# Kernel optimization log

Measured on AMD Instinct MI355X. Metric: run time of the kernel, lower is better.

Reference implementation:

```python
import jax, jax.numpy as jnp
import numpy as np


def _euclidean_cdist(x, q):
    # torch.cdist with p=2: pairwise L2 distances, shape [B, Q]
    x2 = jnp.sum(x * x, axis=-1, keepdims=True)          # [B, 1]
    q2 = jnp.sum(q * q, axis=-1)[None, :]                # [1, Q]
    d2 = x2 + q2 - 2.0 * (x @ q.T)                        # [B, Q]
    return jnp.sqrt(jnp.maximum(d2, 0.0))


def setup_inputs() -> dict:
    key = jax.random.key(0)
    k1, k2 = jax.random.split(key)
    x = jax.random.normal(k1, (1024, 256), dtype=jnp.float32)
    queue = jax.random.normal(k2, (32768, 256), dtype=jnp.float32)
    return {"x": x, "queue": queue}


def reference(x, queue):
    # Queue update: concat then keep the newest max_size rows (queue assumed full)
    max_size = queue.shape[0]
    q = jnp.concatenate([queue, x], axis=0)[-max_size:]   # [Q, F]
    # Distance matrix + top-2 nearest (topk of negated distances)
    d = _euclidean_cdist(x, q)                            # [B, Q]
    _, idx = jax.lax.top_k(-d, 2)                         # [B, 2]
    # Second-nearest neighbor (first is the point itself, dist 0)
    return q[idx[:, 1]]                                   # [B, F]
```

## Files before the change

kernel.cpp:

```cpp
#include <hip/hip_runtime.h>
#include <stdint.h>

#define B_ROWS 1024
#define FEAT   256
#define QSZ    32768
#define SHIFT  1024
#define QX     (QSZ - B_ROWS)
#define NQB    (QSZ / 128)

typedef float  v4f __attribute__((ext_vector_type(4)));
typedef short  v8s __attribute__((ext_vector_type(8)));

struct Top2 { float m1; int j1; float m2; int j2; };

__device__ __forceinline__ bool better(float ma, int ja, float mb, int jb) {
    return (ma < mb) || (ma == mb && ja < jb);
}
__device__ __forceinline__ void t2_insert(Top2& t, float m, int j) {
    if (better(m, j, t.m1, t.j1)) { t.m2 = t.m1; t.j2 = t.j1; t.m1 = m; t.j1 = j; }
    else if (better(m, j, t.m2, t.j2)) { t.m2 = m; t.j2 = j; }
}
__device__ __forceinline__ void t2_merge(Top2& a, const Top2& b) {
    t2_insert(a, b.m1, b.j1); t2_insert(a, b.m2, b.j2);
}
__device__ __forceinline__ float4 t2_pack(const Top2& t) {
    return make_float4(t.m1, __int_as_float(t.j1), t.m2, __int_as_float(t.j2));
}
__device__ __forceinline__ Top2 t2_unpack(float4 v) {
    Top2 t; t.m1 = v.x; t.j1 = __float_as_int(v.y); t.m2 = v.z; t.j2 = __float_as_int(v.w);
    return t;
}
__device__ __forceinline__ Top2 t2_shfl_xor(const Top2& a, int mask) {
    Top2 o;
    o.m1 = __shfl_xor(a.m1, mask, 64);
    o.j1 = __shfl_xor(a.j1, mask, 64);
    o.m2 = __shfl_xor(a.m2, mask, 64);
    o.j2 = __shfl_xor(a.j2, mask, 64);
    return o;
}

__device__ __forceinline__ const float* q_row_ptr(int j, const float* x, const float* queue) {
    return (j < QX) ? (queue + (size_t)(j + SHIFT) * FEAT) : (x + (size_t)(j - QX) * FEAT);
}

__device__ __forceinline__ unsigned short f2bf(float f) {
    uint32_t u = __float_as_uint(f);
    uint32_t r = u + 0x7FFFu + ((u >> 16) & 1u);
    return (unsigned short)(r >> 16);
}

__device__ __forceinline__ void lds_load16(const void* g, void* l) {
    __builtin_amdgcn_global_load_lds(
        (const __attribute__((address_space(1))) uint32_t*)g,
        (__attribute__((address_space(3))) uint32_t*)l, 16, 0, 0);
}

__global__ __launch_bounds__(256) void convert_kernel(const float* __restrict__ x,
                                                      const float* __restrict__ queue,
                                                      unsigned short* __restrict__ q_bf,
                                                      float* __restrict__ q2) {
    int wave = threadIdx.x >> 6, lane = threadIdx.x & 63;
    int j = blockIdx.x * 4 + wave;
    const float4* row = (const float4*)q_row_ptr(j, x, queue);
    float4 v = row[lane];
    float s = v.x * v.x + v.y * v.y + v.z * v.z + v.w * v.w;
#pragma unroll
    for (int off = 32; off; off >>= 1) s += __shfl_xor(s, off, 64);
    if (lane == 0) q2[j] = s;
    ushort4 h;
    h.x = f2bf(v.x); h.y = f2bf(v.y); h.z = f2bf(v.z); h.w = f2bf(v.w);
    ((ushort4*)q_bf)[(size_t)j * 64 + lane] = h;
}

__global__ __launch_bounds__(256, 3) void nn_mfma(const unsigned short* __restrict__ q_bf,
                                                  const float* __restrict__ q2,
                                                  float4* __restrict__ partials) {
    __shared__ unsigned short As[128 * 64];
    __shared__ unsigned short Bs[128 * 64];

    const int t    = threadIdx.x;
    const int w    = t >> 6, lane = t & 63;
    const int wm   = w >> 1, wn = w & 1;
    const int quad = lane >> 4, l16 = lane & 15;
    const int gy   = blockIdx.x;
    const int gx   = blockIdx.y;

    const unsigned short* x_bf = q_bf + (size_t)QX * FEAT;

    v4f acc[4][4];
#pragma unroll
    for (int a = 0; a < 4; ++a)
#pragma unroll
        for (int b = 0; b < 4; ++b) acc[a][b] = (v4f)0.0f;

    const int srow = lane >> 3;
    const int sg   = (lane & 7) ^ (srow & 7);

    for (int c = 0; c < 4; ++c) {
        __syncthreads();
#pragma unroll
        for (int kk = 0; kk < 4; ++kk) {
            int row = w * 32 + kk * 8 + srow;
            const unsigned short* ga = x_bf + (size_t)(gx * 128 + row) * FEAT + c * 64 + sg * 8;
            const unsigned short* gb = q_bf + (size_t)(gy * 128 + row) * FEAT + c * 64 + sg * 8;
            lds_load16(ga, &As[(w * 32 + kk * 8) * 64]);
            lds_load16(gb, &Bs[(w * 32 + kk * 8) * 64]);
        }
        __syncthreads();
#pragma unroll
        for (int ks = 0; ks < 2; ++ks) {
            v8s fa[4], fb[4];
            const int goff  = (((ks * 4 + quad) ^ (l16 & 7)) << 4);
            const int abase = (wm * 64 + l16) * 128 + goff;
            const int bbase = (wn * 64 + l16) * 128 + goff;
#pragma unroll
            for (int tm = 0; tm < 4; ++tm)
                fa[tm] = *(const v8s*)((const char*)As + abase + tm * 2048);
#pragma unroll
            for (int tn = 0; tn < 4; ++tn)
                fb[tn] = *(const v8s*)((const char*)Bs + bbase + tn * 2048);
#pragma unroll
            for (int tm = 0; tm < 4; ++tm)
#pragma unroll
                for (int tn = 0; tn < 4; ++tn)
                    acc[tm][tn] = __builtin_amdgcn_mfma_f32_16x16x32_bf16(fa[tm], fb[tn], acc[tm][tn], 0, 0, 0);
        }
    }

    float q2v[4]; int jcol[4];
#pragma unroll
    for (int tn = 0; tn < 4; ++tn) {
        jcol[tn] = gy * 128 + wn * 64 + tn * 16 + l16;
        q2v[tn]  = q2[jcol[tn]];
    }

    __syncthreads();
    float4* scratch = (float4*)As;
#pragma unroll
    for (int tm = 0; tm < 4; ++tm) {
#pragma unroll
        for (int reg = 0; reg < 4; ++reg) {
            float m0 = q2v[0] - 2.0f * acc[tm][0][reg];
            float m1 = q2v[1] - 2.0f * acc[tm][1][reg];
            float m2 = q2v[2] - 2.0f * acc[tm][2][reg];
            float m3 = q2v[3] - 2.0f * acc[tm][3][reg];
            Top2 tp;
            if (better(m1, jcol[1], m0, jcol[0])) { tp.m1 = m1; tp.j1 = jcol[1]; tp.m2 = m0; tp.j2 = jcol[0]; }
            else                                   { tp.m1 = m0; tp.j1 = jcol[0]; tp.m2 = m1; tp.j2 = jcol[1]; }
            t2_insert(tp, m2, jcol[2]);
            t2_insert(tp, m3, jcol[3]);
#pragma unroll
            for (int mask = 1; mask <= 8; mask <<= 1) t2_merge(tp, t2_shfl_xor(tp, mask));
            if (l16 == 0)
                scratch[(wm * 64 + tm * 16 + quad * 4 + reg) * 2 + wn] = t2_pack(tp);
        }
    }
    __syncthreads();
    if (t < 128) {
        Top2 a = t2_unpack(scratch[t * 2]);
        t2_merge(a, t2_unpack(scratch[t * 2 + 1]));
        partials[(size_t)(gx * 128 + t) * NQB + gy] = t2_pack(a);
    }
}

__global__ __launch_bounds__(256) void nn_finalize(const float* __restrict__ x,
                                                   const float* __restrict__ queue,
                                                   const float* __restrict__ q2,
                                                   const float4* __restrict__ partials,
                                                   float* __restrict__ out) {
    __shared__ float  xs[256];
    __shared__ float4 red[256];
    __shared__ int    list[64];
    __shared__ float  escore[64];
    __shared__ int    s_cnt;
    __shared__ float  s_cut;
    __shared__ int    s_j2;

    const int t = threadIdx.x, i = blockIdx.x;
    const int w = t >> 6, lane = t & 63;

    xs[t] = x[(size_t)i * FEAT + t];
    float4 p = partials[(size_t)i * NQB + t];
    Top2 mine = t2_unpack(p);
    red[t] = p;
    if (t == 0) s_cnt = 0;
    __syncthreads();

    if (w == 0) {
        Top2 a = t2_unpack(red[lane]);
        t2_merge(a, t2_unpack(red[lane + 64]));
        t2_merge(a, t2_unpack(red[lane + 128]));
        t2_merge(a, t2_unpack(red[lane + 192]));
#pragma unroll
        for (int mask = 1; mask <= 32; mask <<= 1) t2_merge(a, t2_shfl_xor(a, mask));
        if (lane == 0) s_cut = a.m2 + 1.0f;
    }
    __syncthreads();
    float cut = s_cut;
    if (mine.m1 <= cut) { int q_ = atomicAdd(&s_cnt, 1); if (q_ < 64) list[q_] = mine.j1; }
    if (mine.m2 <= cut) { int q_ = atomicAdd(&s_cnt, 1); if (q_ < 64) list[q_] = mine.j2; }
    __syncthreads();
    int n = min(s_cnt, 64);

    for (int c = w; c < n; c += 4) {
        int j = list[c];
        const float4* qr = (const float4*)q_row_ptr(j, x, queue);
        float4 qv = qr[lane];
        float4 xv = ((const float4*)xs)[lane];
        float s = qv.x * xv.x + qv.y * xv.y + qv.z * xv.z + qv.w * xv.w;
#pragma unroll
        for (int off = 32; off; off >>= 1) s += __shfl_xor(s, off, 64);
        if (lane == 0) escore[c] = q2[j] - 2.0f * s;
    }
    __syncthreads();
    if (t == 0) {
        Top2 a;
        a.m1 = __builtin_inff(); a.j1 = 0x7FFFFFFF;
        a.m2 = __builtin_inff(); a.j2 = 0x7FFFFFFF;
        for (int c = 0; c < n; ++c) t2_insert(a, escore[c], list[c]);
        s_j2 = a.j2;
    }
    __syncthreads();
    out[(size_t)i * FEAT + t] = q_row_ptr(s_j2, x, queue)[t];
}

extern "C" void kernel_launch(void* const* d_in, const int* in_sizes, int n_in,
                              void* d_out, int out_size, void* d_ws, size_t ws_size,
                              hipStream_t stream) {
    const float* x     = (const float*)d_in[0];
    const float* queue = (const float*)d_in[1];

    unsigned short* q_bf     = (unsigned short*)d_ws;
    float*          q2       = (float*)((char*)d_ws + (16u << 20));
    float4*         partials = (float4*)((char*)d_ws + (17u << 20));

    convert_kernel<<<QSZ / 4, 256, 0, stream>>>(x, queue, q_bf, q2);
    nn_mfma<<<dim3(QSZ / 128, B_ROWS / 128), 256, 0, stream>>>(q_bf, q2, partials);
    nn_finalize<<<B_ROWS, 256, 0, stream>>>(x, queue, q2, partials, (float*)d_out);
}
```

Before: 138.6 us.

## Pack top-2 candidates into sortable uint32 keys with embedded indices

Distance scores are packed into 32-bit keys: the float is order-flipped, truncated to its upper 17 bits, and the lower 15 bits hold the queue index. Top-2 selection then reduces to integer min/max with no branches. The operand roles are also swapped so queue rows map to MFMA rows, which lets each lane reduce over its 16 accumulator registers before only two cross-lane shuffles. Partials shrink from float4 to uint2, and the wider candidate margin in finalize is meant to absorb the truncation error. In exchange, the 15-bit index field fits only because the queue has 32768 rows, and coarser scores may admit more candidates for exact re-scoring, capped at 64.

```diff
diff --git a/kernel.cpp b/kernel.cpp
--- a/kernel.cpp
+++ b/kernel.cpp
@@ -6,37 +6,37 @@
 #define QSZ    32768
 #define SHIFT  1024
 #define QX     (QSZ - B_ROWS)
-#define NQB    (QSZ / 128)
+#define NQB    256
+#define NXB    8
+#define MARGIN 8.0f
 
 typedef float  v4f __attribute__((ext_vector_type(4)));
 typedef short  v8s __attribute__((ext_vector_type(8)));
 
+__device__ __forceinline__ uint32_t key_flip(uint32_t u) {
+    return u ^ ((uint32_t)((int32_t)u >> 31) | 0x80000000u);
+}
+__device__ __forceinline__ float key_m(uint32_t k) {
+    uint32_t u = k & 0xFFFF8000u;
+    u = (u & 0x80000000u) ? (u ^ 0x80000000u) : ~u;
+    return __uint_as_float(u);
+}
+__device__ __forceinline__ void k2_insert(uint32_t& k1, uint32_t& k2, uint32_t key) {
+    uint32_t hi = max(k1, key); k1 = min(k1, key); k2 = min(k2, hi);
+}
+__device__ __forceinline__ uint2 k2_merge(uint2 a, uint2 b) {
+    uint32_t hi = max(a.x, b.x);
+    uint2 r; r.x = min(a.x, b.x); r.y = min(min(a.y, b.y), hi);
+    return r;
+}
+
 struct Top2 { float m1; int j1; float m2; int j2; };
-
 __device__ __forceinline__ bool better(float ma, int ja, float mb, int jb) {
     return (ma < mb) || (ma == mb && ja < jb);
 }
 __device__ __forceinline__ void t2_insert(Top2& t, float m, int j) {
     if (better(m, j, t.m1, t.j1)) { t.m2 = t.m1; t.j2 = t.j1; t.m1 = m; t.j1 = j; }
     else if (better(m, j, t.m2, t.j2)) { t.m2 = m; t.j2 = j; }
-}
-__device__ __forceinline__ void t2_merge(Top2& a, const Top2& b) {
-    t2_insert(a, b.m1, b.j1); t2_insert(a, b.m2, b.j2);
-}
-__device__ __forceinline__ float4 t2_pack(const Top2& t) {
-    return make_float4(t.m1, __int_as_float(t.j1), t.m2, __int_as_float(t.j2));
-}
-__device__ __forceinline__ Top2 t2_unpack(float4 v) {
-    Top2 t; t.m1 = v.x; t.j1 = __float_as_int(v.y); t.m2 = v.z; t.j2 = __float_as_int(v.w);
-    return t;
-}
-__device__ __forceinline__ Top2 t2_shfl_xor(const Top2& a, int mask) {
-    Top2 o;
-    o.m1 = __shfl_xor(a.m1, mask, 64);
-    o.j1 = __shfl_xor(a.j1, mask, 64);
-    o.m2 = __shfl_xor(a.m2, mask, 64);
-    o.j2 = __shfl_xor(a.j2, mask, 64);
-    return o;
 }
 
 __device__ __forceinline__ const float* q_row_ptr(int j, const float* x, const float* queue) {
@@ -74,9 +74,11 @@
 
 __global__ __launch_bounds__(256, 3) void nn_mfma(const unsigned short* __restrict__ q_bf,
                                                   const float* __restrict__ q2,
-                                                  float4* __restrict__ partials) {
+                                                  uint2* __restrict__ partials) {
     __shared__ unsigned short As[128 * 64];
     __shared__ unsigned short Bs[128 * 64];
+    __shared__ float sq2[128];
+    __shared__ uint2 scr[128][2];
 
     const int t    = threadIdx.x;
     const int w    = t >> 6, lane = t & 63;
@@ -87,6 +89,8 @@
 
     const unsigned short* x_bf = q_bf + (size_t)QX * FEAT;
 
+    if (t < 128) sq2[t] = q2[gy * 128 + t];
+
     v4f acc[4][4];
 #pragma unroll
     for (int a = 0; a < 4; ++a)
@@ -94,15 +98,15 @@
         for (int b = 0; b < 4; ++b) acc[a][b] = (v4f)0.0f;
 
     const int srow = lane >> 3;
-    const int sg   = (lane & 7) ^ (srow & 7);
+    const int sg   = (lane & 7) ^ srow;
 
     for (int c = 0; c < 4; ++c) {
         __syncthreads();
 #pragma unroll
         for (int kk = 0; kk < 4; ++kk) {
             int row = w * 32 + kk * 8 + srow;
-            const unsigned short* ga = x_bf + (size_t)(gx * 128 + row) * FEAT + c * 64 + sg * 8;
-            const unsigned short* gb = q_bf + (size_t)(gy * 128 + row) * FEAT + c * 64 + sg * 8;
+            const unsigned short* ga = q_bf + (size_t)(gy * 128 + row) * FEAT + c * 64 + sg * 8;
+            const unsigned short* gb = x_bf + (size_t)(gx * 128 + row) * FEAT + c * 64 + sg * 8;
             lds_load16(ga, &As[(w * 32 + kk * 8) * 64]);
             lds_load16(gb, &Bs[(w * 32 + kk * 8) * 64]);
         }
@@ -127,78 +131,92 @@
         }
     }
 
-    float q2v[4]; int jcol[4];
+    float q2r[4][4];
+#pragma unroll
+    for (int tm = 0; tm < 4; ++tm) {
+        v4f qq = *(const v4f*)&sq2[wm * 64 + tm * 16 + quad * 4];
+#pragma unroll
+        for (int r = 0; r < 4; ++r) q2r[tm][r] = qq[r];
+    }
+    const int jbase = gy * 128 + wm * 64 + quad * 4;
+
+    uint2 best[4];
 #pragma unroll
     for (int tn = 0; tn < 4; ++tn) {
-        jcol[tn] = gy * 128 + wn * 64 + tn * 16 + l16;
-        q2v[tn]  = q2[jcol[tn]];
-    }
-
-    __syncthreads();
-    float4* scratch = (float4*)As;
-#pragma unroll
-    for (int tm = 0; tm < 4; ++tm) {
-#pragma unroll
-        for (int reg = 0; reg < 4; ++reg) {
-            float m0 = q2v[0] - 2.0f * acc[tm][0][reg];
-            float m1 = q2v[1] - 2.0f * acc[tm][1][reg];
-            float m2 = q2v[2] - 2.0f * acc[tm][2][reg];
-            float m3 = q2v[3] - 2.0f * acc[tm][3][reg];
-            Top2 tp;
-            if (better(m1, jcol[1], m0, jcol[0])) { tp.m1 = m1; tp.j1 = jcol[1]; tp.m2 = m0; tp.j2 = jcol[0]; }
-            else                                   { tp.m1 = m0; tp.j1 = jcol[0]; tp.m2 = m1; tp.j2 = jcol[1]; }
-            t2_insert(tp, m2, jcol[2]);
-            t2_insert(tp, m3, jcol[3]);
-#pragma unroll
-            for (int mask = 1; mask <= 8; mask <<= 1) t2_merge(tp, t2_shfl_xor(tp, mask));
-            if (l16 == 0)
-                scratch[(wm * 64 + tm * 16 + quad * 4 + reg) * 2 + wn] = t2_pack(tp);
-        }
+        uint32_t k1 = 0xFFFFFFFFu, k2 = 0xFFFFFFFFu;
+#pragma unroll
+        for (int tm = 0; tm < 4; ++tm)
+#pragma unroll
+            for (int r = 0; r < 4; ++r) {
+                float m = fmaf(-2.0f, acc[tm][tn][r], q2r[tm][r]);
+                uint32_t u = key_flip(__float_as_uint(m));
+                uint32_t key = (u & 0xFFFF8000u) | (uint32_t)(jbase + tm * 16 + r);
+                k2_insert(k1, k2, key);
+            }
+#pragma unroll
+        for (int mask = 16; mask <= 32; mask <<= 1) {
+            uint32_t o1 = __shfl_xor(k1, mask, 64);
+            uint32_t o2 = __shfl_xor(k2, mask, 64);
+            uint32_t hi = max(k1, o1);
+            k1 = min(k1, o1);
+            k2 = min(min(k2, o2), hi);
+        }
+        best[tn] = make_uint2(k1, k2);
+    }
+    if (quad == 0) {
+#pragma unroll
+        for (int tn = 0; tn < 4; ++tn) scr[wn * 64 + tn * 16 + l16][wm] = best[tn];
     }
     __syncthreads();
     if (t < 128) {
-        Top2 a = t2_unpack(scratch[t * 2]);
-        t2_merge(a, t2_unpack(scratch[t * 2 + 1]));
-        partials[(size_t)(gx * 128 + t) * NQB + gy] = t2_pack(a);
+        uint2 r = k2_merge(scr[t][0], scr[t][1]);
+        partials[(size_t)(gx * 128 + t) * NQB + gy] = r;
     }
 }
 
 __global__ __launch_bounds__(256) void nn_finalize(const float* __restrict__ x,
                                                    const float* __restrict__ queue,
                                                    const float* __restrict__ q2,
-                                                   const float4* __restrict__ partials,
+                                                   const uint2* __restrict__ partials,
                                                    float* __restrict__ out) {
-    __shared__ float  xs[256];
-    __shared__ float4 red[256];
-    __shared__ int    list[64];
-    __shared__ float  escore[64];
-    __shared__ int    s_cnt;
-    __shared__ float  s_cut;
-    __shared__ int    s_j2;
+    __shared__ float    xs[256];
+    __shared__ uint2    red[256];
+    __shared__ int      list[64];
+    __shared__ float    escore[64];
+    __shared__ int      s_cnt;
+    __shared__ uint32_t s_kcut;
+    __shared__ int      s_j2;
 
     const int t = threadIdx.x, i = blockIdx.x;
     const int w = t >> 6, lane = t & 63;
 
     xs[t] = x[(size_t)i * FEAT + t];
-    float4 p = partials[(size_t)i * NQB + t];
-    Top2 mine = t2_unpack(p);
+    uint2 p = partials[(size_t)i * NQB + t];
     red[t] = p;
     if (t == 0) s_cnt = 0;
     __syncthreads();
 
     if (w == 0) {
-        Top2 a = t2_unpack(red[lane]);
-        t2_merge(a, t2_unpack(red[lane + 64]));
-        t2_merge(a, t2_unpack(red[lane + 128]));
-        t2_merge(a, t2_unpack(red[lane + 192]));
-#pragma unroll
-        for (int mask = 1; mask <= 32; mask <<= 1) t2_merge(a, t2_shfl_xor(a, mask));
-        if (lane == 0) s_cut = a.m2 + 1.0f;
-    }
-    __syncthreads();
-    float cut = s_cut;
-    if (mine.m1 <= cut) { int q_ = atomicAdd(&s_cnt, 1); if (q_ < 64) list[q_] = mine.j1; }
-    if (mine.m2 <= cut) { int q_ = atomicAdd(&s_cnt, 1); if (q_ < 64) list[q_] = mine.j2; }
+        uint2 a = red[lane];
+        a = k2_merge(a, red[lane + 64]);
+        a = k2_merge(a, red[lane + 128]);
+        a = k2_merge(a, red[lane + 192]);
+#pragma unroll
+        for (int mask = 1; mask <= 32; mask <<= 1) {
+            uint2 o;
+            o.x = __shfl_xor(a.x, mask, 64);
+            o.y = __shfl_xor(a.y, mask, 64);
+            a = k2_merge(a, o);
+        }
+        if (lane == 0) {
+            float cutf = key_m(a.y) + MARGIN;
+            s_kcut = key_flip(__float_as_uint(cutf)) | 0x7FFFu;
+        }
+    }
+    __syncthreads();
+    uint32_t kcut = s_kcut;
+    if (p.x <= kcut) { int q_ = atomicAdd(&s_cnt, 1); if (q_ < 64) list[q_] = (int)(p.x & 0x7FFFu); }
+    if (p.y <= kcut) { int q_ = atomicAdd(&s_cnt, 1); if (q_ < 64) list[q_] = (int)(p.y & 0x7FFFu); }
     __syncthreads();
     int n = min(s_cnt, 64);
 
@@ -232,9 +250,9 @@
 
     unsigned short* q_bf     = (unsigned short*)d_ws;
     float*          q2       = (float*)((char*)d_ws + (16u << 20));
-    float4*         partials = (float4*)((char*)d_ws + (17u << 20));
+    uint2*          partials = (uint2*)((char*)d_ws + (17u << 20));
 
     convert_kernel<<<QSZ / 4, 256, 0, stream>>>(x, queue, q_bf, q2);
-    nn_mfma<<<dim3(QSZ / 128, B_ROWS / 128), 256, 0, stream>>>(q_bf, q2, partials);
+    nn_mfma<<<dim3(NQB, NXB), 256, 0, stream>>>(q_bf, q2, partials);
     nn_finalize<<<B_ROWS, 256, 0, stream>>>(x, queue, q2, partials, (float*)d_out);
 }
```

Measured after the change: 111.9 us. 19.3% less time.
